# Kernel optimization log

Measured on AMD Instinct MI355X. Metric: run time of the kernel, lower is better.

The kernel has to match this reference:

```python
import jax, jax.numpy as jnp
import numpy as np

DIM = 2048
NUM_HEADS = 16
NUM_KV_HEADS = 4
HEAD_DIM = DIM // NUM_HEADS  # 128


def apply_rotary_emb(x, freqs_cis):
    # x: [b, s, h, head_dim]; freqs_cis: [s, head_dim//2, 2]
    b, s, h, d = x.shape
    xs = x.reshape(b, s, h, d // 2, 2)
    fc = freqs_cis.reshape(1, s, 1, d // 2, 2)
    real = xs[..., 0] * fc[..., 0] - xs[..., 1] * fc[..., 1]
    imag = xs[..., 1] * fc[..., 0] + xs[..., 0] * fc[..., 1]
    return jnp.stack([real, imag], axis=-1).reshape(b, s, h, d)


def setup_inputs() -> dict:
    key = jax.random.key(0)
    k1, k2, k3, k4 = jax.random.split(key, 4)
    b, s = 2, 2048
    x = jax.random.normal(k1, (b, s, DIM), dtype=jnp.float32)
    freqs_cis = jax.random.uniform(k2, (s, HEAD_DIM // 2, 2), dtype=jnp.float32)
    total_kv_dim = (NUM_HEADS + 2 * NUM_KV_HEADS) * HEAD_DIM  # 3072
    wqkv = jax.random.normal(k3, (total_kv_dim, DIM), dtype=jnp.float32) * (DIM ** -0.5)
    wo = jax.random.normal(k4, (DIM, DIM), dtype=jnp.float32) * (DIM ** -0.5)
    return {"x": x, "freqs_cis": freqs_cis, "wqkv": wqkv, "wo": wo}


def reference(x, freqs_cis, wqkv, wo):
    b, s, _ = x.shape
    kv_size = NUM_KV_HEADS * HEAD_DIM
    qkv = jnp.einsum('bsd,od->bso', x, wqkv)
    xq = qkv[..., :DIM].reshape(b, s, NUM_HEADS, HEAD_DIM)
    xk = qkv[..., DIM:DIM + kv_size].reshape(b, s, NUM_KV_HEADS, HEAD_DIM)
    xv = qkv[..., DIM + kv_size:].reshape(b, s, NUM_KV_HEADS, HEAD_DIM)
    xq = apply_rotary_emb(xq, freqs_cis)
    xk = apply_rotary_emb(xk, freqs_cis)
    # -> [b, h, s, d]
    q = xq.transpose(0, 2, 1, 3)
    k = xk.transpose(0, 2, 1, 3)
    v = xv.transpose(0, 2, 1, 3)
    rep = NUM_HEADS // NUM_KV_HEADS
    k = jnp.repeat(k, rep, axis=1)
    v = jnp.repeat(v, rep, axis=1)
    scale = HEAD_DIM ** -0.5
    scores = jnp.einsum('bhqd,bhkd->bhqk', q, k) * scale
    causal = jnp.tril(jnp.ones((s, s), dtype=bool))
    scores = jnp.where(causal[None, None], scores, jnp.finfo(scores.dtype).min)
    attn = jax.nn.softmax(scores, axis=-1)
    out = jnp.einsum('bhqk,bhkd->bhqd', attn, v)
    out = out.transpose(0, 2, 1, 3).reshape(b, s, DIM)
    return jnp.einsum('bsd,od->bso', out, wo)
```

## Files before the change

kernel.cpp:

```cpp
#include <hip/hip_runtime.h>
#include <stdint.h>

typedef uint16_t u16;
typedef float f32x4 __attribute__((ext_vector_type(4)));
typedef short bf16x8 __attribute__((ext_vector_type(8)));

constexpr int NB = 2, NS = 2048, ND = 2048, NH = 16, NKVH = 4, HDIM = 128;
constexpr int QKVD = 3072;
constexpr int TOK = NB * NS;
constexpr float SM_SCALE = 0.08838834764831845f;
constexpr float LOG2E = 1.4426950408889634f;
constexpr float QK_SCALE = SM_SCALE * LOG2E;

#define WAITVM(N) asm volatile("s_waitcnt vmcnt(" #N ")" ::: "memory")
#define WAITLGKM0 asm volatile("s_waitcnt lgkmcnt(0)" ::: "memory")
#define MEMFENCE asm volatile("" ::: "memory")

__device__ __forceinline__ u16 f2bf(float f) {
  union { float f; uint32_t u; } v; v.f = f;
  return (u16)((v.u + 0x7fffu + ((v.u >> 16) & 1u)) >> 16);
}
__device__ __forceinline__ uint32_t cvt_pk_bf16(float lo, float hi) {
  uint32_t r;
  asm("v_cvt_pk_bf16_f32 %0, %1, %2" : "=v"(r) : "v"(lo), "v"(hi));
  return r;
}

__device__ __forceinline__ void gload_lds16(const void* g, void* l) {
  void* gv = const_cast<void*>(g);
  __builtin_amdgcn_global_load_lds(
      (__attribute__((address_space(1))) void*)gv,
      (__attribute__((address_space(3))) void*)l, 16, 0, 0);
}

__global__ __launch_bounds__(256)
void cvt3(const float* __restrict__ x, const float* __restrict__ wq,
          const float* __restrict__ wo, u16* __restrict__ xb,
          u16* __restrict__ wqb, u16* __restrict__ wob) {
  constexpr int N1 = TOK * ND / 4, N2 = QKVD * ND / 4, N3 = ND * ND / 4;
  int i = blockIdx.x * 256 + threadIdx.x;
  const float* src; u16* dst; int j;
  if (i < N1)              { src = x;  dst = xb;  j = i; }
  else if (i < N1 + N2)    { src = wq; dst = wqb; j = i - N1; }
  else if (i < N1 + N2 + N3){ src = wo; dst = wob; j = i - N1 - N2; }
  else return;
  const float4 v = reinterpret_cast<const float4*>(src)[j];
  union { u16 h[4]; uint2 u; } o;
  o.h[0] = f2bf(v.x); o.h[1] = f2bf(v.y); o.h[2] = f2bf(v.z); o.h[3] = f2bf(v.w);
  reinterpret_cast<uint2*>(dst)[j] = o.u;
}

template <int MODE>
__global__ __launch_bounds__(256, 2)
void gemm_bt(const u16* __restrict__ A, const u16* __restrict__ Bm,
             void* __restrict__ Cv, int M, int N, int K,
             const float* __restrict__ fc, u16* __restrict__ Qb,
             u16* __restrict__ Kb, u16* __restrict__ Vt) {
  __shared__ u16 As[2][128 * 32];
  __shared__ u16 Bs[2][128 * 32];
  const int tid = threadIdx.x;
  const int lane = tid & 63;
  const int wid = tid >> 6;
  const int wr = wid >> 1, wc = wid & 1;
  const int rowA0 = blockIdx.y * 128, colB0 = blockIdx.x * 128;
  const int lr = lane & 15;
  const int lg = lane >> 4;
  const int lk = lg * 8;
  const char* Ab = (const char*)A;
  const char* Bb = (const char*)Bm;
  f32x4 acc[4][4] = {};
  const int nkt = K >> 5;

  auto STAGE = [&](int kt, int buf) {
#pragma unroll
    for (int p = 0; p < 2; ++p) {
      int o = p * 4096 + tid * 16;
      int row = o >> 6, kb = o & 63;
      gload_lds16(Ab + ((size_t)(rowA0 + row) * K + kt * 32) * 2 + kb, (char*)As[buf] + o);
      gload_lds16(Bb + ((size_t)(colB0 + row) * K + kt * 32) * 2 + kb, (char*)Bs[buf] + o);
    }
  };

  STAGE(0, 0);
  for (int kt = 0; kt < nkt; ++kt) {
    const int cur = kt & 1;
    if (kt + 1 < nkt) { STAGE(kt + 1, cur ^ 1); WAITVM(4); }
    else              { WAITVM(0); }
    __builtin_amdgcn_s_barrier();
    MEMFENCE;
    const u16* Ac = As[cur];
    const u16* Bc = Bs[cur];
    bf16x8 af[4], bfr[4];
#pragma unroll
    for (int m = 0; m < 4; ++m)
      af[m] = *(const bf16x8*)&Ac[(wr * 64 + m * 16 + lr) * 32 + lk];
#pragma unroll
    for (int n = 0; n < 4; ++n)
      bfr[n] = *(const bf16x8*)&Bc[(wc * 64 + n * 16 + lr) * 32 + lk];
    __builtin_amdgcn_s_setprio(1);
#pragma unroll
    for (int m = 0; m < 4; ++m)
#pragma unroll
      for (int n = 0; n < 4; ++n)
        acc[m][n] = __builtin_amdgcn_mfma_f32_16x16x32_bf16(af[m], bfr[n], acc[m][n], 0, 0, 0);
    __builtin_amdgcn_s_setprio(0);
    WAITLGKM0;
    __builtin_amdgcn_s_barrier();
    MEMFENCE;
  }

  if (MODE == 0) {
#pragma unroll
    for (int m = 0; m < 4; ++m) {
      int row0 = rowA0 + wr * 64 + m * 16 + lg * 4;
#pragma unroll
      for (int n = 0; n < 4; ++n) {
        int col = colB0 + wc * 64 + n * 16 + lr;
#pragma unroll
        for (int r = 0; r < 4; ++r)
          ((float*)Cv)[(size_t)(row0 + r) * N + col] = acc[m][n][r];
      }
    }
  } else {
    const int colblk = colB0 >> 7;
#pragma unroll
    for (int m = 0; m < 4; ++m) {
      int row0 = rowA0 + wr * 64 + m * 16 + lg * 4;
      int b_ = row0 >> 11;
      int s0 = row0 & 2047;
#pragma unroll
      for (int n = 0; n < 4; ++n) {
        int d = wc * 64 + n * 16 + lr;
        f32x4 v = acc[m][n];
        if (colblk < 20) {
          f32x4 pw;
#pragma unroll
          for (int r = 0; r < 4; ++r) pw[r] = __shfl_xor(v[r], 1, 64);
          int p = d >> 1;
          const bool ev = !(d & 1);
#pragma unroll
          for (int r = 0; r < 4; ++r) {
            int st = s0 + r;
            float c = fc[(st * 64 + p) * 2];
            float sn = fc[(st * 64 + p) * 2 + 1];
            float res = ev ? (v[r] * c - pw[r] * sn) : (v[r] * c + pw[r] * sn);
            if (colblk < 16)
              Qb[((size_t)(b_ * NH + colblk) * NS + st) * HDIM + d] = f2bf(res);
            else
              Kb[((size_t)(b_ * NKVH + (colblk - 16)) * NS + st) * HDIM + d] =
                  f2bf(res * QK_SCALE);
          }
        } else {
          int kv = colblk - 20;
          union { u16 h[4]; uint2 u; } o;
#pragma unroll
          for (int r = 0; r < 4; ++r) o.h[r] = f2bf(v[r]);
          *(uint2*)&Vt[((size_t)(b_ * NKVH + kv) * HDIM + d) * NS + s0] = o.u;
        }
      }
    }
  }
}

__global__ __launch_bounds__(512, 2)
void flash_attn(const u16* __restrict__ Qb, const u16* __restrict__ Kb,
                const u16* __restrict__ Vt, u16* __restrict__ Ob) {
  __shared__ u16 Ks[2][64 * 128];
  __shared__ u16 Vs[2][128 * 64];
  const int idx = blockIdx.x;
  const int grp = idx & 7;
  const int b = grp >> 2, kvh = grp & 3;
  const int rest = idx >> 3;
  const int h = kvh * 4 + (rest & 3);
  const int pair = rest >> 2;
  const int tid = threadIdx.x, lane = tid & 63, w = tid >> 6;
  const int lr = lane & 15, lg = lane >> 4;

  bf16x8 ones;
#pragma unroll
  for (int j = 0; j < 8; ++j) ones[j] = (short)0x3F80;

  const char* Kbase = (const char*)(Kb + (size_t)(b * NKVH + kvh) * NS * HDIM);
  const char* Vbase = (const char*)(Vt + (size_t)(b * NKVH + kvh) * HDIM * NS);

  auto STAGE = [&](int kt, int buf) {
#pragma unroll
    for (int p = 0; p < 2; ++p) {
      int o = p * 8192 + tid * 16;
      int krow = o >> 8, kwb = o & 255;
      gload_lds16(Kbase + (size_t)(kt * 64 + krow) * 256 + (kwb ^ ((krow & 7) << 4)),
                  (char*)Ks[buf] + o);
      int vrow = o >> 7, vwb = o & 127;
      gload_lds16(Vbase + (size_t)vrow * (NS * 2) + kt * 128 + (vwb ^ ((vrow & 7) << 4)),
                  (char*)Vs[buf] + o);
    }
  };

  for (int t = 0; t < 2; ++t) {
    const int qt = t ? (NS / 128 - 1 - pair) : pair;

    bf16x8 aq[4];
    {
      const u16* Qrow = Qb + ((size_t)(b * NH + h) * NS + qt * 128 + w * 16 + lr) * HDIM;
#pragma unroll
      for (int ks = 0; ks < 4; ++ks)
        aq[ks] = *(const bf16x8*)(Qrow + ks * 32 + lg * 8);
    }

    float mrun = -1e30f;
    f32x4 accl = {0.f, 0.f, 0.f, 0.f};
    f32x4 acco[8] = {};

    const int qglob = qt * 128 + w * 16 + lr;
    const int qrow0 = qt * 128 + w * 16 + lg * 4;
    const int wave_min_row = qt * 128 + w * 16;
    const int wave_max_row = wave_min_row + 15;

    const int ktmax = 2 * qt + 1;
    STAGE(0, 0);
    for (int kt = 0; kt <= ktmax; ++kt) {
      const int cur = kt & 1;
      if (kt < ktmax) { STAGE(kt + 1, cur ^ 1); WAITVM(4); }
      else            { WAITVM(0); }
      __builtin_amdgcn_s_barrier();
      MEMFENCE;

      if (kt * 64 <= wave_max_row) {
        const char* Kc = (const char*)Ks[cur];
        const char* Vc = (const char*)Vs[cur];

        f32x4 accs[4] = {};
        __builtin_amdgcn_s_setprio(1);
#pragma unroll
        for (int n = 0; n < 4; ++n) {
          int row = n * 16 + lr;
          int swz = (row & 7) << 4;
#pragma unroll
          for (int ks = 0; ks < 4; ++ks) {
            int cb = (ks * 32 + lg * 8) * 2;
            bf16x8 bk = *(const bf16x8*)(Kc + row * 256 + (cb ^ swz));
            accs[n] = __builtin_amdgcn_mfma_f32_16x16x32_bf16(bk, aq[ks], accs[n], 0, 0, 0);
          }
        }
        __builtin_amdgcn_s_setprio(0);

        if (kt * 64 + 63 > wave_min_row) {
#pragma unroll
          for (int n = 0; n < 4; ++n) {
            int kbase = kt * 64 + n * 16 + lg * 4;
#pragma unroll
            for (int r = 0; r < 4; ++r)
              if (kbase + r > qglob) accs[n][r] = -1e30f;
          }
        }

        float pmax = fmaxf(fmaxf(fmaxf(accs[0][0], accs[0][1]), fmaxf(accs[0][2], accs[0][3])),
                           fmaxf(fmaxf(accs[1][0], accs[1][1]), fmaxf(accs[1][2], accs[1][3])));
        pmax = fmaxf(pmax,
               fmaxf(fmaxf(fmaxf(accs[2][0], accs[2][1]), fmaxf(accs[2][2], accs[2][3])),
                     fmaxf(fmaxf(accs[3][0], accs[3][1]), fmaxf(accs[3][2], accs[3][3]))));
        pmax = fmaxf(pmax, __shfl_xor(pmax, 16, 64));
        pmax = fmaxf(pmax, __shfl_xor(pmax, 32, 64));

        bool ok = (pmax <= mrun + 8.f);
        if (!__all(ok)) {
          float mnew = fmaxf(mrun, pmax);
          float alpha = exp2f(mrun - mnew);
          mrun = mnew;
          float alr[4];
#pragma unroll
          for (int r = 0; r < 4; ++r)
            alr[r] = __shfl(alpha, lg * 4 + r, 64);
#pragma unroll
          for (int r = 0; r < 4; ++r) accl[r] *= alr[r];
#pragma unroll
          for (int n2 = 0; n2 < 8; ++n2)
#pragma unroll
            for (int r = 0; r < 4; ++r) acco[n2][r] *= alr[r];
        }

        uint32_t w0[4], w1[4];
#pragma unroll
        for (int n = 0; n < 4; ++n) {
          float p0 = exp2f(accs[n][0] - mrun);
          float p1 = exp2f(accs[n][1] - mrun);
          float p2 = exp2f(accs[n][2] - mrun);
          float p3 = exp2f(accs[n][3] - mrun);
          w0[n] = cvt_pk_bf16(p0, p1);
          w1[n] = cvt_pk_bf16(p2, p3);
        }

        const int s1 = ((lg & 1) << 5) | lr;
        const int s2 = s1 + 16;
        uint32_t F[4][4];
#pragma unroll
        for (int n = 0; n < 4; ++n) {
          F[n][0] = __shfl((int)w0[n], s1, 64);
          F[n][1] = __shfl((int)w1[n], s1, 64);
          F[n][2] = __shfl((int)w0[n], s2, 64);
          F[n][3] = __shfl((int)w1[n], s2, 64);
        }
        const bool hi = (lg & 2);
        bf16x8 pa[2];
#pragma unroll
        for (int ks = 0; ks < 2; ++ks) {
          union { uint32_t d[4]; bf16x8 v; } u;
#pragma unroll
          for (int j = 0; j < 4; ++j)
            u.d[j] = hi ? F[ks * 2 + 1][j] : F[ks * 2][j];
          pa[ks] = u.v;
        }

        __builtin_amdgcn_s_setprio(1);
#pragma unroll
        for (int ks = 0; ks < 2; ++ks) {
          int cb = (ks * 32 + lg * 8) * 2;
#pragma unroll
          for (int n2 = 0; n2 < 8; ++n2) {
            int d = n2 * 16 + lr;
            bf16x8 bv = *(const bf16x8*)(Vc + d * 128 + (cb ^ ((d & 7) << 4)));
            acco[n2] = __builtin_amdgcn_mfma_f32_16x16x32_bf16(pa[ks], bv, acco[n2], 0, 0, 0);
          }
          accl = __builtin_amdgcn_mfma_f32_16x16x32_bf16(pa[ks], ones, accl, 0, 0, 0);
        }
        __builtin_amdgcn_s_setprio(0);
      }
      WAITLGKM0;
      __builtin_amdgcn_s_barrier();
      MEMFENCE;
    }

#pragma unroll
    for (int n2 = 0; n2 < 8; ++n2) {
      int d = n2 * 16 + lr;
#pragma unroll
      for (int r = 0; r < 4; ++r) {
        int q = qrow0 + r;
        Ob[((size_t)b * NS + q) * ND + h * HDIM + d] = f2bf(acco[n2][r] / accl[r]);
      }
    }
  }
}

extern "C" void kernel_launch(void* const* d_in, const int* in_sizes, int n_in,
                              void* d_out, int out_size, void* d_ws, size_t ws_size,
                              hipStream_t stream) {
  const float* x = (const float*)d_in[0];
  const float* fc = (const float*)d_in[1];
  const float* wqkv = (const float*)d_in[2];
  const float* wo = (const float*)d_in[3];
  float* out = (float*)d_out;
  char* ws = (char*)d_ws;
  size_t off = 0;
  u16* xb = (u16*)(ws + off);    off += (size_t)TOK * ND * 2;
  u16* wqkvb = (u16*)(ws + off); off += (size_t)QKVD * ND * 2;
  u16* wob = (u16*)(ws + off);   off += (size_t)ND * ND * 2;
  u16* Qb = (u16*)(ws + off);    off += (size_t)NB * NH * NS * HDIM * 2;
  u16* Kb = (u16*)(ws + off);    off += (size_t)NB * NKVH * NS * HDIM * 2;
  u16* Vtb = (u16*)(ws + off);   off += (size_t)NB * NKVH * NS * HDIM * 2;
  u16* attnb = (u16*)(ws + off); off += (size_t)TOK * ND * 2;
  (void)ws_size; (void)in_sizes; (void)n_in; (void)out_size;

  constexpr int CVTN = (TOK * ND + QKVD * ND + ND * ND) / 4;
  cvt3<<<CVTN / 256, 256, 0, stream>>>(x, wqkv, wo, xb, wqkvb, wob);
  gemm_bt<2><<<dim3(QKVD / 128, TOK / 128), 256, 0, stream>>>(
      xb, wqkvb, nullptr, TOK, QKVD, ND, fc, Qb, Kb, Vtb);
  flash_attn<<<dim3(256), 512, 0, stream>>>(Qb, Kb, Vtb, attnb);
  gemm_bt<0><<<dim3(ND / 128, TOK / 128), 256, 0, stream>>>(
      attnb, wob, out, TOK, ND, ND, nullptr, nullptr, nullptr, nullptr);
}
```

Measured before the change: 213.8 us.

## Split flash attention into one q-tile per block with 32-key tiles

Drops the paired causal q-tile scheme (each block handling qt and its mirror) and launches 512 blocks, each owning a single 128-row q-tile, ordered so the heaviest tiles go first. The K/V stage shrinks to 32 keys, which halves LDS use, and launch bounds rise to 4 blocks per CU for higher occupancy. The cost is twice as many loop iterations and barriers per key span, and the V swizzle changes to fit the narrower tile. Load balance now depends on the hardware scheduler rather than on the explicit pairing.

```diff
diff --git a/kernel.cpp b/kernel.cpp
--- a/kernel.cpp
+++ b/kernel.cpp
@@ -162,17 +162,17 @@
   }
 }
 
-__global__ __launch_bounds__(512, 2)
+__global__ __launch_bounds__(512, 4)
 void flash_attn(const u16* __restrict__ Qb, const u16* __restrict__ Kb,
                 const u16* __restrict__ Vt, u16* __restrict__ Ob) {
-  __shared__ u16 Ks[2][64 * 128];
-  __shared__ u16 Vs[2][128 * 64];
+  __shared__ u16 Ks[2][32 * 128];
+  __shared__ u16 Vs[2][128 * 32];
   const int idx = blockIdx.x;
-  const int grp = idx & 7;
-  const int b = grp >> 2, kvh = grp & 3;
-  const int rest = idx >> 3;
+  const int qt = (NS / 128 - 1) - (idx >> 5);
+  const int rest = idx & 31;
+  const int b = rest >> 4;
+  const int kvh = (rest >> 2) & 3;
   const int h = kvh * 4 + (rest & 3);
-  const int pair = rest >> 2;
   const int tid = threadIdx.x, lane = tid & 63, w = tid >> 6;
   const int lr = lane & 15, lg = lane >> 4;
 
@@ -184,160 +184,144 @@
   const char* Vbase = (const char*)(Vt + (size_t)(b * NKVH + kvh) * HDIM * NS);
 
   auto STAGE = [&](int kt, int buf) {
-#pragma unroll
-    for (int p = 0; p < 2; ++p) {
-      int o = p * 8192 + tid * 16;
-      int krow = o >> 8, kwb = o & 255;
-      gload_lds16(Kbase + (size_t)(kt * 64 + krow) * 256 + (kwb ^ ((krow & 7) << 4)),
-                  (char*)Ks[buf] + o);
-      int vrow = o >> 7, vwb = o & 127;
-      gload_lds16(Vbase + (size_t)vrow * (NS * 2) + kt * 128 + (vwb ^ ((vrow & 7) << 4)),
-                  (char*)Vs[buf] + o);
-    }
+    int o = tid * 16;
+    int krow = o >> 8, kwb = o & 255;
+    gload_lds16(Kbase + (size_t)(kt * 32 + krow) * 256 + (kwb ^ ((krow & 7) << 4)),
+                (char*)Ks[buf] + o);
+    int vrow = o >> 6, vwb = o & 63;
+    gload_lds16(Vbase + (size_t)vrow * (NS * 2) + kt * 64 + (vwb ^ ((vrow & 3) << 4)),
+                (char*)Vs[buf] + o);
   };
 
-  for (int t = 0; t < 2; ++t) {
-    const int qt = t ? (NS / 128 - 1 - pair) : pair;
-
-    bf16x8 aq[4];
-    {
-      const u16* Qrow = Qb + ((size_t)(b * NH + h) * NS + qt * 128 + w * 16 + lr) * HDIM;
-#pragma unroll
-      for (int ks = 0; ks < 4; ++ks)
-        aq[ks] = *(const bf16x8*)(Qrow + ks * 32 + lg * 8);
-    }
-
-    float mrun = -1e30f;
-    f32x4 accl = {0.f, 0.f, 0.f, 0.f};
-    f32x4 acco[8] = {};
-
-    const int qglob = qt * 128 + w * 16 + lr;
-    const int qrow0 = qt * 128 + w * 16 + lg * 4;
-    const int wave_min_row = qt * 128 + w * 16;
-    const int wave_max_row = wave_min_row + 15;
-
-    const int ktmax = 2 * qt + 1;
-    STAGE(0, 0);
-    for (int kt = 0; kt <= ktmax; ++kt) {
-      const int cur = kt & 1;
-      if (kt < ktmax) { STAGE(kt + 1, cur ^ 1); WAITVM(4); }
-      else            { WAITVM(0); }
-      __builtin_amdgcn_s_barrier();
-      MEMFENCE;
-
-      if (kt * 64 <= wave_max_row) {
-        const char* Kc = (const char*)Ks[cur];
-        const char* Vc = (const char*)Vs[cur];
-
-        f32x4 accs[4] = {};
-        __builtin_amdgcn_s_setprio(1);
-#pragma unroll
-        for (int n = 0; n < 4; ++n) {
-          int row = n * 16 + lr;
-          int swz = (row & 7) << 4;
-#pragma unroll
-          for (int ks = 0; ks < 4; ++ks) {
-            int cb = (ks * 32 + lg * 8) * 2;
-            bf16x8 bk = *(const bf16x8*)(Kc + row * 256 + (cb ^ swz));
-            accs[n] = __builtin_amdgcn_mfma_f32_16x16x32_bf16(bk, aq[ks], accs[n], 0, 0, 0);
-          }
+  bf16x8 aq[4];
+  {
+    const u16* Qrow = Qb + ((size_t)(b * NH + h) * NS + qt * 128 + w * 16 + lr) * HDIM;
+#pragma unroll
+    for (int ks = 0; ks < 4; ++ks)
+      aq[ks] = *(const bf16x8*)(Qrow + ks * 32 + lg * 8);
+  }
+
+  float mrun = -1e30f;
+  f32x4 accl = {0.f, 0.f, 0.f, 0.f};
+  f32x4 acco[8] = {};
+
+  const int qglob = qt * 128 + w * 16 + lr;
+  const int qrow0 = qt * 128 + w * 16 + lg * 4;
+  const int wave_min_row = qt * 128 + w * 16;
+  const int wave_max_row = wave_min_row + 15;
+
+  const int ktmax = 4 * qt + 3;
+  STAGE(0, 0);
+  for (int kt = 0; kt <= ktmax; ++kt) {
+    const int cur = kt & 1;
+    if (kt < ktmax) { STAGE(kt + 1, cur ^ 1); WAITVM(2); }
+    else            { WAITVM(0); }
+    __builtin_amdgcn_s_barrier();
+    MEMFENCE;
+
+    if (kt * 32 <= wave_max_row) {
+      const char* Kc = (const char*)Ks[cur];
+      const char* Vc = (const char*)Vs[cur];
+
+      f32x4 accs[2] = {};
+      __builtin_amdgcn_s_setprio(1);
+#pragma unroll
+      for (int n = 0; n < 2; ++n) {
+        int row = n * 16 + lr;
+        int swz = (row & 7) << 4;
+#pragma unroll
+        for (int ks = 0; ks < 4; ++ks) {
+          int cb = (ks * 32 + lg * 8) * 2;
+          bf16x8 bk = *(const bf16x8*)(Kc + row * 256 + (cb ^ swz));
+          accs[n] = __builtin_amdgcn_mfma_f32_16x16x32_bf16(bk, aq[ks], accs[n], 0, 0, 0);
         }
-        __builtin_amdgcn_s_setprio(0);
-
-        if (kt * 64 + 63 > wave_min_row) {
-#pragma unroll
-          for (int n = 0; n < 4; ++n) {
-            int kbase = kt * 64 + n * 16 + lg * 4;
-#pragma unroll
-            for (int r = 0; r < 4; ++r)
-              if (kbase + r > qglob) accs[n][r] = -1e30f;
-          }
+      }
+      __builtin_amdgcn_s_setprio(0);
+
+      if (kt * 32 + 31 > wave_min_row) {
+#pragma unroll
+        for (int n = 0; n < 2; ++n) {
+          int kbase = kt * 32 + n * 16 + lg * 4;
+#pragma unroll
+          for (int r = 0; r < 4; ++r)
+            if (kbase + r > qglob) accs[n][r] = -1e30f;
         }
-
-        float pmax = fmaxf(fmaxf(fmaxf(accs[0][0], accs[0][1]), fmaxf(accs[0][2], accs[0][3])),
-                           fmaxf(fmaxf(accs[1][0], accs[1][1]), fmaxf(accs[1][2], accs[1][3])));
-        pmax = fmaxf(pmax,
-               fmaxf(fmaxf(fmaxf(accs[2][0], accs[2][1]), fmaxf(accs[2][2], accs[2][3])),
-                     fmaxf(fmaxf(accs[3][0], accs[3][1]), fmaxf(accs[3][2], accs[3][3]))));
-        pmax = fmaxf(pmax, __shfl_xor(pmax, 16, 64));
-        pmax = fmaxf(pmax, __shfl_xor(pmax, 32, 64));
-
-        bool ok = (pmax <= mrun + 8.f);
-        if (!__all(ok)) {
-          float mnew = fmaxf(mrun, pmax);
-          float alpha = exp2f(mrun - mnew);
-          mrun = mnew;
-          float alr[4];
-#pragma unroll
-          for (int r = 0; r < 4; ++r)
-            alr[r] = __shfl(alpha, lg * 4 + r, 64);
-#pragma unroll
-          for (int r = 0; r < 4; ++r) accl[r] *= alr[r];
-#pragma unroll
-          for (int n2 = 0; n2 < 8; ++n2)
-#pragma unroll
-            for (int r = 0; r < 4; ++r) acco[n2][r] *= alr[r];
+      }
+
+      float pmax = fmaxf(fmaxf(fmaxf(accs[0][0], accs[0][1]), fmaxf(accs[0][2], accs[0][3])),
+                         fmaxf(fmaxf(accs[1][0], accs[1][1]), fmaxf(accs[1][2], accs[1][3])));
+      pmax = fmaxf(pmax, __shfl_xor(pmax, 16, 64));
+      pmax = fmaxf(pmax, __shfl_xor(pmax, 32, 64));
+
+      bool ok = (pmax <= mrun + 8.f);
+      if (!__all(ok)) {
+        float mnew = fmaxf(mrun, pmax);
+        float alpha = exp2f(mrun - mnew);
+        mrun = mnew;
+        float alr[4];
+#pragma unroll
+        for (int r = 0; r < 4; ++r)
+          alr[r] = __shfl(alpha, lg * 4 + r, 64);
+#pragma unroll
+        for (int r = 0; r < 4; ++r) accl[r] *= alr[r];
+#pragma unroll
+        for (int n2 = 0; n2 < 8; ++n2)
+#pragma unroll
+          for (int r = 0; r < 4; ++r) acco[n2][r] *= alr[r];
+      }
+
+      uint32_t w0[2], w1[2];
+#pragma unroll
+      for (int n = 0; n < 2; ++n) {
+        w0[n] = cvt_pk_bf16(exp2f(accs[n][0] - mrun), exp2f(accs[n][1] - mrun));
+        w1[n] = cvt_pk_bf16(exp2f(accs[n][2] - mrun), exp2f(accs[n][3] - mrun));
+      }
+
+      const int s1 = ((lg & 1) << 5) | lr;
+      const int s2 = s1 + 16;
+      uint32_t F[2][4];
+#pragma unroll
+      for (int n = 0; n < 2; ++n) {
+        F[n][0] = __shfl((int)w0[n], s1, 64);
+        F[n][1] = __shfl((int)w1[n], s1, 64);
+        F[n][2] = __shfl((int)w0[n], s2, 64);
+        F[n][3] = __shfl((int)w1[n], s2, 64);
+      }
+      const bool hi = (lg & 2);
+      bf16x8 pa;
+      {
+        union { uint32_t d[4]; bf16x8 v; } u;
+#pragma unroll
+        for (int j = 0; j < 4; ++j)
+          u.d[j] = hi ? F[1][j] : F[0][j];
+        pa = u.v;
+      }
+
+      __builtin_amdgcn_s_setprio(1);
+      {
+        int cb = lg * 16;
+#pragma unroll
+        for (int n2 = 0; n2 < 8; ++n2) {
+          int d = n2 * 16 + lr;
+          bf16x8 bv = *(const bf16x8*)(Vc + d * 64 + (cb ^ ((d & 3) << 4)));
+          acco[n2] = __builtin_amdgcn_mfma_f32_16x16x32_bf16(pa, bv, acco[n2], 0, 0, 0);
         }
-
-        uint32_t w0[4], w1[4];
-#pragma unroll
-        for (int n = 0; n < 4; ++n) {
-          float p0 = exp2f(accs[n][0] - mrun);
-          float p1 = exp2f(accs[n][1] - mrun);
-          float p2 = exp2f(accs[n][2] - mrun);
-          float p3 = exp2f(accs[n][3] - mrun);
-          w0[n] = cvt_pk_bf16(p0, p1);
-          w1[n] = cvt_pk_bf16(p2, p3);
-        }
-
-        const int s1 = ((lg & 1) << 5) | lr;
-        const int s2 = s1 + 16;
-        uint32_t F[4][4];
-#pragma unroll
-        for (int n = 0; n < 4; ++n) {
-          F[n][0] = __shfl((int)w0[n], s1, 64);
-          F[n][1] = __shfl((int)w1[n], s1, 64);
-          F[n][2] = __shfl((int)w0[n], s2, 64);
-          F[n][3] = __shfl((int)w1[n], s2, 64);
-        }
-        const bool hi = (lg & 2);
-        bf16x8 pa[2];
-#pragma unroll
-        for (int ks = 0; ks < 2; ++ks) {
-          union { uint32_t d[4]; bf16x8 v; } u;
-#pragma unroll
-          for (int j = 0; j < 4; ++j)
-            u.d[j] = hi ? F[ks * 2 + 1][j] : F[ks * 2][j];
-          pa[ks] = u.v;
-        }
-
-        __builtin_amdgcn_s_setprio(1);
-#pragma unroll
-        for (int ks = 0; ks < 2; ++ks) {
-          int cb = (ks * 32 + lg * 8) * 2;
-#pragma unroll
-          for (int n2 = 0; n2 < 8; ++n2) {
-            int d = n2 * 16 + lr;
-            bf16x8 bv = *(const bf16x8*)(Vc + d * 128 + (cb ^ ((d & 7) << 4)));
-            acco[n2] = __builtin_amdgcn_mfma_f32_16x16x32_bf16(pa[ks], bv, acco[n2], 0, 0, 0);
-          }
-          accl = __builtin_amdgcn_mfma_f32_16x16x32_bf16(pa[ks], ones, accl, 0, 0, 0);
-        }
-        __builtin_amdgcn_s_setprio(0);
-      }
-      WAITLGKM0;
-      __builtin_amdgcn_s_barrier();
-      MEMFENCE;
-    }
-
-#pragma unroll
-    for (int n2 = 0; n2 < 8; ++n2) {
-      int d = n2 * 16 + lr;
-#pragma unroll
-      for (int r = 0; r < 4; ++r) {
-        int q = qrow0 + r;
-        Ob[((size_t)b * NS + q) * ND + h * HDIM + d] = f2bf(acco[n2][r] / accl[r]);
-      }
+        accl = __builtin_amdgcn_mfma_f32_16x16x32_bf16(pa, ones, accl, 0, 0, 0);
+      }
+      __builtin_amdgcn_s_setprio(0);
+    }
+    WAITLGKM0;
+    __builtin_amdgcn_s_barrier();
+    MEMFENCE;
+  }
+
+#pragma unroll
+  for (int n2 = 0; n2 < 8; ++n2) {
+    int d = n2 * 16 + lr;
+#pragma unroll
+    for (int r = 0; r < 4; ++r) {
+      int q = qrow0 + r;
+      Ob[((size_t)b * NS + q) * ND + h * HDIM + d] = f2bf(acco[n2][r] / accl[r]);
     }
   }
 }
@@ -365,7 +349,7 @@
   cvt3<<<CVTN / 256, 256, 0, stream>>>(x, wqkv, wo, xb, wqkvb, wob);
   gemm_bt<2><<<dim3(QKVD / 128, TOK / 128), 256, 0, stream>>>(
       xb, wqkvb, nullptr, TOK, QKVD, ND, fc, Qb, Kb, Vtb);
-  flash_attn<<<dim3(256), 512, 0, stream>>>(Qb, Kb, Vtb, attnb);
+  flash_attn<<<dim3(512), 512, 0, stream>>>(Qb, Kb, Vtb, attnb);
   gemm_bt<0><<<dim3(ND / 128, TOK / 128), 256, 0, stream>>>(
       attnb, wob, out, TOK, ND, ND, nullptr, nullptr, nullptr, nullptr);
 }
```

New measurement: 260.0 us. +21.6%, slower.
